# Performance work log

Hardware: AMD Instinct MI355X
Metric: run time of the kernel (lower is better)

## Reference

```python
import jax, jax.numpy as jnp
import numpy as np

B, P, DE, DD, DA = 256, 196, 2048, 512, 512

def setup_inputs() -> dict:
    key = jax.random.key(0)
    ks = jax.random.split(key, 8)
    s_enc = 1.0 / np.sqrt(DE)
    s_dec = 1.0 / np.sqrt(DD)
    s_att = 1.0 / np.sqrt(DA)
    return {
        "encoder_out": jax.random.normal(ks[0], (B, P, DE), dtype=jnp.float32),
        "decoder_hidden": jax.random.normal(ks[1], (B, DD), dtype=jnp.float32),
        "W_enc": jax.random.uniform(ks[2], (DE, DA), jnp.float32, -s_enc, s_enc),
        "b_enc": jax.random.uniform(ks[3], (DA,), jnp.float32, -s_enc, s_enc),
        "W_dec": jax.random.uniform(ks[4], (DD, DA), jnp.float32, -s_dec, s_dec),
        "b_dec": jax.random.uniform(ks[5], (DA,), jnp.float32, -s_dec, s_dec),
        "W_full": jax.random.uniform(ks[6], (DA, 1), jnp.float32, -s_att, s_att),
        "b_full": jax.random.uniform(ks[7], (1,), jnp.float32, -s_att, s_att),
    }

def reference(encoder_out, decoder_hidden, W_enc, b_enc, W_dec, b_dec, W_full, b_full):
    # att1: [B,P,DA]; att2: [B,DA]
    att1 = jnp.einsum('bpe,ea->bpa', encoder_out, W_enc) + b_enc
    att2 = decoder_hidden @ W_dec + b_dec
    # broadcast add + relu + project to scalar score per position
    att = jnp.einsum('bpa,a->bp', jax.nn.relu(att1 + att2[:, None, :]), W_full[:, 0]) + b_full[0]
    alpha = jax.nn.softmax(att, axis=1)  # [B,P]
    context_vector = jnp.einsum('bpe,bp->be', encoder_out, alpha)  # [B,DE]
    return (context_vector, alpha)
```

## Files before the change

kernel.cpp:

```cpp
#include <hip/hip_runtime.h>
#include <hip/hip_bf16.h>
#include <cstddef>

#define B_   256
#define P_   196
#define DE_  2048
#define DD_  512
#define DA_  512
#define M_   (B_*P_)

#define BM   64
#define KT   32
#define NKT  (DE_/KT)

typedef __attribute__((ext_vector_type(4))) float f32x4;
typedef __attribute__((ext_vector_type(8))) short s16x8;

static __device__ __forceinline__ short f2bf(float x) {
    __hip_bfloat16 h = __float2bfloat16(x);
    return *reinterpret_cast<short*>(&h);
}

__global__ __launch_bounds__(256) void pack_wenc(
        const float* __restrict__ W, __hip_bfloat16* __restrict__ out) {
    __shared__ float lds[KT][DA_];
    const int kt = blockIdx.x;
    const int t  = threadIdx.x;
#pragma unroll
    for (int i = 0; i < 64; ++i) {
        int e = i * 256 + t;
        int k = e >> 9, n = e & 511;
        lds[k][n] = W[(size_t)(kt * KT + k) * DA_ + n];
    }
    __syncthreads();
    short* o = reinterpret_cast<short*>(out) + (size_t)kt * (32 * 64 * 8);
#pragma unroll
    for (int i = 0; i < 8; ++i) {
        int idx  = i * 256 + t;
        int gf   = idx >> 6;
        int lane = idx & 63;
        int g = lane >> 4, c = lane & 15;
        s16x8 w;
#pragma unroll
        for (int j = 0; j < 8; ++j)
            w[j] = f2bf(lds[g * 8 + j][gf * 16 + c]);
        *reinterpret_cast<s16x8*>(o + (size_t)idx * 8) = w;
    }
}

__global__ __launch_bounds__(512) void att2_kernel(
        const float* __restrict__ dh, const float* __restrict__ W_dec,
        const float* __restrict__ b_dec, const float* __restrict__ b_enc,
        float* __restrict__ att2p) {
    __shared__ float s_dh[DD_];
    const int b = blockIdx.x;
    const int a = threadIdx.x;
    s_dh[a] = dh[(size_t)b * DD_ + a];
    __syncthreads();
    float acc = 0.f;
#pragma unroll 8
    for (int k = 0; k < DD_; ++k)
        acc += s_dh[k] * W_dec[(size_t)k * DA_ + a];
    att2p[(size_t)b * DA_ + a] = acc + b_dec[a] + b_enc[a];
}

__global__ __launch_bounds__(256, 3) void gemm_att(
        const float* __restrict__ enc, const __hip_bfloat16* __restrict__ Bp,
        const float* __restrict__ att2p, const float* __restrict__ Wfull,
        float* __restrict__ att0, float* __restrict__ att1) {
    __shared__ __hip_bfloat16 a_lds0[BM * KT];
    __shared__ __hip_bfloat16 a_lds1[BM * KT];
    __shared__ float red[BM][4];

    const int tid  = threadIdx.x;
    const int wave = tid >> 6;
    const int lane = tid & 63;
    const int g    = lane >> 4;
    const int c    = lane & 15;

    const int p   = blockIdx.x;
    const int mt_ = (p >> 4) * 8 + (p & 7);
    const int nh  = (p >> 3) & 1;
    const int block_row = mt_ * BM;

    const int slot8 = (g ^ ((c >> 1) & 3)) * 8;

    const int ar = tid >> 2;
    const int aq = tid & 3;
    const int a_woff = ar * KT + (aq ^ ((ar >> 1) & 3)) * 8;
    const float* ap = enc + (size_t)(block_row + ar) * DE_ + aq * 8;

    const s16x8* bp = reinterpret_cast<const s16x8*>(Bp)
                    + ((size_t)(nh * 16 + wave * 4)) * 64 + lane;

    f32x4 acc[4][4] = {};
    f32x4 pX0, pX1, pY0, pY1;
    s16x8 bfX[4], bfY[4];

#define ISSUE_A(v0, v1, T) do {                                          \
        const int tt_ = (T) > 63 ? 63 : (T);                             \
        v0 = *reinterpret_cast<const f32x4*>(ap + tt_ * KT);             \
        v1 = *reinterpret_cast<const f32x4*>(ap + tt_ * KT + 4);         \
    } while (0)

#define ISSUE_B(dst, T) do {                                             \
        _Pragma("unroll")                                                \
        for (int nt_ = 0; nt_ < 4; ++nt_)                                \
            dst[nt_] = bp[((size_t)(T) * 32 + nt_) * 64];                \
    } while (0)

#define STORE_A(dst, v0, v1) do {                                        \
        s16x8 w_;                                                        \
        w_[0]=f2bf((v0).x); w_[1]=f2bf((v0).y); w_[2]=f2bf((v0).z); w_[3]=f2bf((v0).w); \
        w_[4]=f2bf((v1).x); w_[5]=f2bf((v1).y); w_[6]=f2bf((v1).z); w_[7]=f2bf((v1).w); \
        *reinterpret_cast<s16x8*>((dst) + a_woff) = w_;                  \
    } while (0)

#define FRAGS_MFMA(abuf, bfr) do {                                       \
        s16x8 af[4];                                                     \
        _Pragma("unroll")                                                \
        for (int mt2 = 0; mt2 < 4; ++mt2)                                \
            af[mt2] = *reinterpret_cast<const s16x8*>((abuf) + (mt2*16 + c) * KT + slot8); \
        _Pragma("unroll")                                                \
        for (int nt2 = 0; nt2 < 4; ++nt2)                                \
            _Pragma("unroll")                                            \
            for (int mt2 = 0; mt2 < 4; ++mt2)                            \
                acc[mt2][nt2] = __builtin_amdgcn_mfma_f32_16x16x32_bf16( \
                                    af[mt2], bfr[nt2], acc[mt2][nt2], 0, 0, 0); \
    } while (0)

#define BAR() do {                                                       \
        asm volatile("s_waitcnt lgkmcnt(0)" ::: "memory");               \
        __builtin_amdgcn_s_barrier();                                    \
        __builtin_amdgcn_sched_barrier(0);                               \
    } while (0)

    ISSUE_A(pX0, pX1, 0);
    ISSUE_A(pY0, pY1, 1);
    ISSUE_B(bfX, 0);
    STORE_A(a_lds0, pX0, pX1);
    ISSUE_A(pX0, pX1, 2);
    ISSUE_B(bfY, 1);
    BAR();

#pragma clang loop unroll(disable)
    for (int t = 0; t < 62; t += 2) {
        STORE_A(a_lds1, pY0, pY1);
        ISSUE_A(pY0, pY1, t + 3);
        FRAGS_MFMA(a_lds0, bfX);
        ISSUE_B(bfX, t + 2);
        BAR();
        STORE_A(a_lds0, pX0, pX1);
        ISSUE_A(pX0, pX1, t + 4);
        FRAGS_MFMA(a_lds1, bfY);
        ISSUE_B(bfY, t + 3);
        BAR();
    }
    STORE_A(a_lds1, pY0, pY1);
    FRAGS_MFMA(a_lds0, bfX);
    BAR();
    FRAGS_MFMA(a_lds1, bfY);

    const int b0    = block_row / P_;
    const int b1    = min(b0 + 1, B_ - 1);
    const int split = (b0 + 1) * P_;
    const int ncol0 = nh * 256 + wave * 64;
    float wf[4], a20[4], a21[4];
#pragma unroll
    for (int nt = 0; nt < 4; ++nt) {
        const int n = ncol0 + nt * 16 + c;
        wf[nt]  = Wfull[n];
        a20[nt] = att2p[(size_t)b0 * DA_ + n];
        a21[nt] = att2p[(size_t)b1 * DA_ + n];
    }
#pragma unroll
    for (int mt = 0; mt < 4; ++mt) {
#pragma unroll
        for (int q = 0; q < 4; ++q) {
            const int row_local = mt * 16 + g * 4 + q;
            const int R = block_row + row_local;
            const bool hi = (R >= split);
            float s = 0.f;
#pragma unroll
            for (int nt = 0; nt < 4; ++nt) {
                float a2 = hi ? a21[nt] : a20[nt];
                float v  = acc[mt][nt][q] + a2;
                v = fmaxf(v, 0.f);
                s += v * wf[nt];
            }
#pragma unroll
            for (int off = 1; off < 16; off <<= 1)
                s += __shfl_xor(s, off, 64);
            if (c == 0) red[row_local][wave] = s;
        }
    }
    __syncthreads();
    if (tid < BM) {
        float t = red[tid][0] + red[tid][1] + red[tid][2] + red[tid][3];
        float* dst = nh ? att1 : att0;
        dst[block_row + tid] = t;
    }
#undef ISSUE_A
#undef ISSUE_B
#undef STORE_A
#undef FRAGS_MFMA
#undef BAR
}

__global__ __launch_bounds__(256) void softmax_kernel(
        const float* __restrict__ att0, const float* __restrict__ att1,
        float* __restrict__ alpha) {
    const int b = blockIdx.x;
    const int t = threadIdx.x;
    __shared__ float sred[4];
    float v = -1e30f;
    if (t < P_) v = att0[(size_t)b * P_ + t] + att1[(size_t)b * P_ + t];
    float m = v;
#pragma unroll
    for (int off = 1; off < 64; off <<= 1) m = fmaxf(m, __shfl_xor(m, off, 64));
    if ((t & 63) == 0) sred[t >> 6] = m;
    __syncthreads();
    const float mall = fmaxf(fmaxf(sred[0], sred[1]), fmaxf(sred[2], sred[3]));
    __syncthreads();
    float e = (t < P_) ? expf(v - mall) : 0.f;
    float s = e;
#pragma unroll
    for (int off = 1; off < 64; off <<= 1) s += __shfl_xor(s, off, 64);
    if ((t & 63) == 0) sred[t >> 6] = s;
    __syncthreads();
    const float stot = sred[0] + sred[1] + sred[2] + sred[3];
    if (t < P_) alpha[(size_t)b * P_ + t] = e / stot;
}

__global__ __launch_bounds__(256) void context_kernel(
        const float* __restrict__ enc, const float* __restrict__ alpha,
        float* __restrict__ ctx) {
    const int b = blockIdx.x;
    const int e = blockIdx.y * 1024 + threadIdx.x * 4;
    __shared__ float s_alpha[P_];
    if (threadIdx.x < P_) s_alpha[threadIdx.x] = alpha[(size_t)b * P_ + threadIdx.x];
    __syncthreads();
    f32x4 acc = {0.f, 0.f, 0.f, 0.f};
    const float* base = enc + (size_t)b * P_ * DE_ + e;
#pragma unroll 4
    for (int p = 0; p < P_; ++p) {
        f32x4 v = *reinterpret_cast<const f32x4*>(base + (size_t)p * DE_);
        acc += s_alpha[p] * v;
    }
    *reinterpret_cast<f32x4*>(ctx + (size_t)b * DE_ + e) = acc;
}

extern "C" void kernel_launch(void* const* d_in, const int* in_sizes, int n_in,
                              void* d_out, int out_size, void* d_ws, size_t ws_size,
                              hipStream_t stream) {
    const float* enc    = (const float*)d_in[0];
    const float* dh     = (const float*)d_in[1];
    const float* W_enc  = (const float*)d_in[2];
    const float* b_enc  = (const float*)d_in[3];
    const float* W_dec  = (const float*)d_in[4];
    const float* b_dec  = (const float*)d_in[5];
    const float* W_full = (const float*)d_in[6];

    float* out       = (float*)d_out;
    float* ctx_out   = out;
    float* alpha_out = out + (size_t)B_ * DE_;

    char* ws = (char*)d_ws;
    __hip_bfloat16* Bp = (__hip_bfloat16*)ws;
    float* att2p = (float*)(ws + 2u * 1024 * 1024);
    float* att0  = (float*)(ws + 2u * 1024 * 1024 + 512u * 1024);
    float* att1  = att0 + M_;

    pack_wenc     <<<NKT,            256, 0, stream>>>(W_enc, Bp);
    att2_kernel   <<<B_,             512, 0, stream>>>(dh, W_dec, b_dec, b_enc, att2p);
    gemm_att      <<<2 * (M_ / BM),  256, 0, stream>>>(enc, Bp, att2p, W_full, att0, att1);
    softmax_kernel<<<B_,             256, 0, stream>>>(att0, att1, alpha_out);
    context_kernel<<<dim3(B_, 2),    256, 0, stream>>>(enc, alpha_out, ctx_out);
}
```

Before: 279.8 us.

## Stream fp32 A tiles directly into a 4-stage LDS ring via global_load_lds

Replaces register-staged A loading (global load, bf16 convert, LDS store) with direct global-to-LDS 16-byte loads of raw fp32 into a four-buffer ring. Synchronisation becomes a vmcnt-based wait plus barrier, so loads run two stages ahead. This is meant to cut VGPR staging and instruction overhead and deepen the prefetch. The cost is four times the A LDS footprint, doubled LDS read traffic, and the bf16 conversion repeated by every wave at fragment-read time.

```diff
diff --git a/kernel.cpp b/kernel.cpp
--- a/kernel.cpp
+++ b/kernel.cpp
@@ -20,6 +20,10 @@
     __hip_bfloat16 h = __float2bfloat16(x);
     return *reinterpret_cast<short*>(&h);
 }
+
+#define GLOAD_LDS16(g, l) __builtin_amdgcn_global_load_lds( \
+    (const __attribute__((address_space(1))) void*)(g),     \
+    (__attribute__((address_space(3))) void*)(l), 16, 0, 0)
 
 __global__ __launch_bounds__(256) void pack_wenc(
         const float* __restrict__ W, __hip_bfloat16* __restrict__ out) {
@@ -68,8 +72,7 @@
         const float* __restrict__ enc, const __hip_bfloat16* __restrict__ Bp,
         const float* __restrict__ att2p, const float* __restrict__ Wfull,
         float* __restrict__ att0, float* __restrict__ att1) {
-    __shared__ __hip_bfloat16 a_lds0[BM * KT];
-    __shared__ __hip_bfloat16 a_lds1[BM * KT];
+    __shared__ float a_lds[4][BM * KT];
     __shared__ float red[BM][4];
 
     const int tid  = threadIdx.x;
@@ -83,44 +86,47 @@
     const int nh  = (p >> 3) & 1;
     const int block_row = mt_ * BM;
 
-    const int slot8 = (g ^ ((c >> 1) & 3)) * 8;
-
-    const int ar = tid >> 2;
-    const int aq = tid & 3;
-    const int a_woff = ar * KT + (aq ^ ((ar >> 1) & 3)) * 8;
-    const float* ap = enc + (size_t)(block_row + ar) * DE_ + aq * 8;
+    const int arow  = tid >> 3;
+    const int aslot = (tid & 7) ^ (arow & 7);
+    const float* a_src = enc + (size_t)(block_row + arow) * DE_ + aslot * 4;
+
+    const int ax  = c & 7;
+    const int ao0 = ((2 * g)     ^ ax) * 4;
+    const int ao1 = ((2 * g + 1) ^ ax) * 4;
 
     const s16x8* bp = reinterpret_cast<const s16x8*>(Bp)
                     + ((size_t)(nh * 16 + wave * 4)) * 64 + lane;
 
     f32x4 acc[4][4] = {};
-    f32x4 pX0, pX1, pY0, pY1;
     s16x8 bfX[4], bfY[4];
 
-#define ISSUE_A(v0, v1, T) do {                                          \
+#define ISSUE_A(T) do {                                                  \
         const int tt_ = (T) > 63 ? 63 : (T);                             \
-        v0 = *reinterpret_cast<const f32x4*>(ap + tt_ * KT);             \
-        v1 = *reinterpret_cast<const f32x4*>(ap + tt_ * KT + 4);         \
-    } while (0)
-
-#define ISSUE_B(dst, T) do {                                             \
+        float* d_ = a_lds[(T) & 3];                                      \
+        GLOAD_LDS16(a_src + tt_ * KT,                 &d_[tid * 4]);     \
+        GLOAD_LDS16(a_src + (size_t)32 * DE_ + tt_ * KT, &d_[(256 + tid) * 4]); \
+    } while (0)
+
+#define LOAD_B(dst, T) do {                                              \
+        const int tt_ = (T) > 63 ? 63 : (T);                             \
         _Pragma("unroll")                                                \
-        for (int nt_ = 0; nt_ < 4; ++nt_)                                \
-            dst[nt_] = bp[((size_t)(T) * 32 + nt_) * 64];                \
-    } while (0)
-
-#define STORE_A(dst, v0, v1) do {                                        \
-        s16x8 w_;                                                        \
-        w_[0]=f2bf((v0).x); w_[1]=f2bf((v0).y); w_[2]=f2bf((v0).z); w_[3]=f2bf((v0).w); \
-        w_[4]=f2bf((v1).x); w_[5]=f2bf((v1).y); w_[6]=f2bf((v1).z); w_[7]=f2bf((v1).w); \
-        *reinterpret_cast<s16x8*>((dst) + a_woff) = w_;                  \
-    } while (0)
-
-#define FRAGS_MFMA(abuf, bfr) do {                                       \
+        for (int n_ = 0; n_ < 4; ++n_)                                   \
+            dst[n_] = bp[((size_t)tt_ * 32 + n_) * 64];                  \
+    } while (0)
+
+#define COMPUTE(T, bfr) do {                                             \
+        const float* ab_ = a_lds[(T) & 3];                               \
         s16x8 af[4];                                                     \
         _Pragma("unroll")                                                \
-        for (int mt2 = 0; mt2 < 4; ++mt2)                                \
-            af[mt2] = *reinterpret_cast<const s16x8*>((abuf) + (mt2*16 + c) * KT + slot8); \
+        for (int mt2 = 0; mt2 < 4; ++mt2) {                              \
+            const float* base_ = ab_ + (mt2 * 16 + c) * KT;              \
+            f32x4 v0_ = *reinterpret_cast<const f32x4*>(base_ + ao0);    \
+            f32x4 v1_ = *reinterpret_cast<const f32x4*>(base_ + ao1);    \
+            s16x8 w_;                                                    \
+            w_[0]=f2bf(v0_.x); w_[1]=f2bf(v0_.y); w_[2]=f2bf(v0_.z); w_[3]=f2bf(v0_.w); \
+            w_[4]=f2bf(v1_.x); w_[5]=f2bf(v1_.y); w_[6]=f2bf(v1_.z); w_[7]=f2bf(v1_.w); \
+            af[mt2] = w_;                                                \
+        }                                                                \
         _Pragma("unroll")                                                \
         for (int nt2 = 0; nt2 < 4; ++nt2)                                \
             _Pragma("unroll")                                            \
@@ -129,37 +135,28 @@
                                     af[mt2], bfr[nt2], acc[mt2][nt2], 0, 0, 0); \
     } while (0)
 
-#define BAR() do {                                                       \
-        asm volatile("s_waitcnt lgkmcnt(0)" ::: "memory");               \
+#define WAIT6_BAR() do {                                                 \
+        asm volatile("s_waitcnt vmcnt(6)" ::: "memory");                 \
         __builtin_amdgcn_s_barrier();                                    \
-        __builtin_amdgcn_sched_barrier(0);                               \
-    } while (0)
-
-    ISSUE_A(pX0, pX1, 0);
-    ISSUE_A(pY0, pY1, 1);
-    ISSUE_B(bfX, 0);
-    STORE_A(a_lds0, pX0, pX1);
-    ISSUE_A(pX0, pX1, 2);
-    ISSUE_B(bfY, 1);
-    BAR();
+    } while (0)
+
+    LOAD_B(bfX, 0);
+    ISSUE_A(0);
+    ISSUE_A(1);
+    LOAD_B(bfY, 1);
+    WAIT6_BAR();
 
 #pragma clang loop unroll(disable)
-    for (int t = 0; t < 62; t += 2) {
-        STORE_A(a_lds1, pY0, pY1);
-        ISSUE_A(pY0, pY1, t + 3);
-        FRAGS_MFMA(a_lds0, bfX);
-        ISSUE_B(bfX, t + 2);
-        BAR();
-        STORE_A(a_lds0, pX0, pX1);
-        ISSUE_A(pX0, pX1, t + 4);
-        FRAGS_MFMA(a_lds1, bfY);
-        ISSUE_B(bfY, t + 3);
-        BAR();
-    }
-    STORE_A(a_lds1, pY0, pY1);
-    FRAGS_MFMA(a_lds0, bfX);
-    BAR();
-    FRAGS_MFMA(a_lds1, bfY);
+    for (int t = 0; t < NKT; t += 2) {
+        ISSUE_A(t + 2);
+        COMPUTE(t, bfX);
+        LOAD_B(bfX, t + 2);
+        WAIT6_BAR();
+        ISSUE_A(t + 3);
+        COMPUTE(t + 1, bfY);
+        LOAD_B(bfY, t + 3);
+        WAIT6_BAR();
+    }
 
     const int b0    = block_row / P_;
     const int b1    = min(b0 + 1, B_ - 1);
@@ -179,11 +176,11 @@
         for (int q = 0; q < 4; ++q) {
             const int row_local = mt * 16 + g * 4 + q;
             const int R = block_row + row_local;
-            const bool hi = (R >= split);
+            const bool hiB = (R >= split);
             float s = 0.f;
 #pragma unroll
             for (int nt = 0; nt < 4; ++nt) {
-                float a2 = hi ? a21[nt] : a20[nt];
+                float a2 = hiB ? a21[nt] : a20[nt];
                 float v  = acc[mt][nt][q] + a2;
                 v = fmaxf(v, 0.f);
                 s += v * wf[nt];
@@ -201,10 +198,9 @@
         dst[block_row + tid] = t;
     }
 #undef ISSUE_A
-#undef ISSUE_B
-#undef STORE_A
-#undef FRAGS_MFMA
-#undef BAR
+#undef LOAD_B
+#undef COMPUTE
+#undef WAIT6_BAR
 }
 
 __global__ __launch_bounds__(256) void softmax_kernel(
```

Result: slower. 312.0 us (+11.5%).
